# Performance work log

Hardware: AMD Instinct MI355X
Metric: run time of the kernel (lower is better)

The kernel has to match this reference:

```python
import jax, jax.numpy as jnp
import numpy as np

B, S, C = 2, 4096, 512
H = 8            # num heads
D = C // H       # head dim = 64


def setup_inputs() -> dict:
    key = jax.random.key(0)
    ks = jax.random.split(key, 5)
    s = 0.02
    return {
        "hidden_states": jax.random.normal(ks[0], (B, S, C), dtype=jnp.float32),
        "Wq": jax.random.normal(ks[1], (C, C), dtype=jnp.float32) * s,
        "Wk": jax.random.normal(ks[2], (C, C), dtype=jnp.float32) * s,
        "Wv": jax.random.normal(ks[3], (C, C), dtype=jnp.float32) * s,
        "Wo": jax.random.normal(ks[4], (C, C), dtype=jnp.float32) * s,
        "bo": jnp.zeros((C,), dtype=jnp.float32),
    }


def reference(hidden_states, Wq, Wk, Wv, Wo, bo):
    # Self-attention path of AttnProcessor (encoder_hidden_states=None,
    # no norms, no mask, residual_connection=False, rescale=1.0).
    b, s, c = hidden_states.shape
    scale = jnp.float32(D) ** -0.5
    # QKV projections (Linear, no bias as in diffusers defaults)
    q = hidden_states @ Wq.T   # [b,s,c]
    k = hidden_states @ Wk.T
    v = hidden_states @ Wv.T
    # head_to_batch_dim: [b,s,c] -> [b,s,h,d]
    q = q.reshape(b, s, H, D)
    k = k.reshape(b, s, H, D)
    v = v.reshape(b, s, H, D)
    # get_attention_scores: scaled QK^T + softmax (full O(S^2) matrix, as in source)
    scores = jnp.einsum("bqhd,bkhd->bhqk", q, k) * scale   # [b,h,s,s]
    probs = jax.nn.softmax(scores, axis=-1)
    # bmm with V, batch_to_head_dim
    out = jnp.einsum("bhqk,bkhd->bqhd", probs, v).reshape(b, s, c)
    # to_out[0] (Linear with bias); to_out[1] is Dropout (identity at eval)
    out = out @ Wo.T + bo
    return out
```

## Files before the change

### kernel.cpp

```cpp
#include <hip/hip_runtime.h>
#include <hip/hip_bf16.h>

#define BB 2
#define SS 4096
#define CC 512
#define HH 8
#define DD 64
#define MM (BB*SS)

typedef __bf16 bf16;
typedef __attribute__((ext_vector_type(8))) __bf16 bf16x8;
typedef __attribute__((ext_vector_type(4))) __bf16 bf16x4;
typedef __attribute__((ext_vector_type(4))) float f32x4;

#define LP 72
#define QSCALE 0.18033688f

__device__ __forceinline__ bf16x8 cvt8(const float4 a, const float4 b) {
  bf16x8 r;
  r[0]=(bf16)a.x; r[1]=(bf16)a.y; r[2]=(bf16)a.z; r[3]=(bf16)a.w;
  r[4]=(bf16)b.x; r[5]=(bf16)b.y; r[6]=(bf16)b.z; r[7]=(bf16)b.w;
  return r;
}

__global__ __launch_bounds__(256) void cvt_f32_bf16(
    const float* __restrict__ src, bf16* __restrict__ dst)
{
  size_t e = ((size_t)blockIdx.x * 256 + threadIdx.x) * 8;
  float4 a = ((const float4*)(src + e))[0];
  float4 b = ((const float4*)(src + e))[1];
  *(bf16x8*)(dst + e) = cvt8(a, b);
}

__global__ __launch_bounds__(256) void cvt_w(
    const float* __restrict__ Wq, const float* __restrict__ Wk,
    const float* __restrict__ Wv, bf16* __restrict__ Wb)
{
  size_t e = ((size_t)blockIdx.x * 256 + threadIdx.x) * 8;
  const int tens = (int)(e >> 18);
  const float* src = ((tens == 0) ? Wq : (tens == 1) ? Wk : Wv) + (e & 262143);
  const float sc = (tens == 0) ? QSCALE : 1.f;
  float4 a = ((const float4*)src)[0];
  float4 b = ((const float4*)src)[1];
  bf16x8 r;
  r[0]=(bf16)(a.x*sc); r[1]=(bf16)(a.y*sc); r[2]=(bf16)(a.z*sc); r[3]=(bf16)(a.w*sc);
  r[4]=(bf16)(b.x*sc); r[5]=(bf16)(b.y*sc); r[6]=(bf16)(b.z*sc); r[7]=(bf16)(b.w*sc);
  *(bf16x8*)(Wb + e) = r;
}

__global__ __launch_bounds__(256) void qkv_gemm(
    const bf16* __restrict__ Xb, const bf16* __restrict__ Wb,
    bf16* __restrict__ qp, bf16* __restrict__ kp, bf16* __restrict__ vtp)
{
  __shared__ bf16 Aa[64*LP];
  __shared__ bf16 Ab[64*LP];
  __shared__ bf16 Ba[64*LP];
  __shared__ bf16 Bb[64*LP];
  const int m0  = blockIdx.x * 128;
  const int nf0 = blockIdx.y * 128;
  const int tens = nf0 >> 9;
  const int n0 = nf0 & 511;

  const int t = threadIdx.x;
  const int w = t >> 6;
  const int lane = t & 63;
  const int l15 = lane & 15;
  const int quad = lane >> 4;
  const int srow = t >> 2;
  const int scol = (t & 3) << 4;

  f32x4 acc[2][2][4];
  #pragma unroll
  for (int mi = 0; mi < 2; ++mi)
    #pragma unroll
    for (int ni = 0; ni < 2; ++ni)
      #pragma unroll
      for (int nt = 0; nt < 4; ++nt)
        #pragma unroll
        for (int r = 0; r < 4; ++r) acc[mi][ni][nt][r] = 0.f;

  for (int k0 = 0; k0 < CC; k0 += 64) {
    __syncthreads();
    {
      const bf16* sa = Xb + (size_t)(m0 + srow) * CC + k0 + scol;
      *(bf16x8*)&Aa[srow*LP + scol]     = ((const bf16x8*)sa)[0];
      *(bf16x8*)&Aa[srow*LP + scol + 8] = ((const bf16x8*)sa)[1];
      const bf16* sb = Xb + (size_t)(m0 + 64 + srow) * CC + k0 + scol;
      *(bf16x8*)&Ab[srow*LP + scol]     = ((const bf16x8*)sb)[0];
      *(bf16x8*)&Ab[srow*LP + scol + 8] = ((const bf16x8*)sb)[1];
      const bf16* s1 = Wb + (size_t)(nf0 + srow) * CC + k0 + scol;
      *(bf16x8*)&Ba[srow*LP + scol]     = ((const bf16x8*)s1)[0];
      *(bf16x8*)&Ba[srow*LP + scol + 8] = ((const bf16x8*)s1)[1];
      const bf16* s2 = Wb + (size_t)(nf0 + 64 + srow) * CC + k0 + scol;
      *(bf16x8*)&Bb[srow*LP + scol]     = ((const bf16x8*)s2)[0];
      *(bf16x8*)&Bb[srow*LP + scol + 8] = ((const bf16x8*)s2)[1];
    }
    __syncthreads();
    #pragma unroll
    for (int c = 0; c < 2; ++c) {
      bf16x8 afa = *(const bf16x8*)&Aa[(w*16 + l15)*LP + c*32 + quad*8];
      bf16x8 afb = *(const bf16x8*)&Ab[(w*16 + l15)*LP + c*32 + quad*8];
      #pragma unroll
      for (int nt = 0; nt < 4; ++nt) {
        bf16x8 ba = *(const bf16x8*)&Ba[(nt*16 + l15)*LP + c*32 + quad*8];
        bf16x8 bb = *(const bf16x8*)&Bb[(nt*16 + l15)*LP + c*32 + quad*8];
        acc[0][0][nt] = __builtin_amdgcn_mfma_f32_16x16x32_bf16(afa, ba, acc[0][0][nt], 0, 0, 0);
        acc[1][0][nt] = __builtin_amdgcn_mfma_f32_16x16x32_bf16(afb, ba, acc[1][0][nt], 0, 0, 0);
        acc[0][1][nt] = __builtin_amdgcn_mfma_f32_16x16x32_bf16(afa, bb, acc[0][1][nt], 0, 0, 0);
        acc[1][1][nt] = __builtin_amdgcn_mfma_f32_16x16x32_bf16(afb, bb, acc[1][1][nt], 0, 0, 0);
      }
    }
  }

  bf16* plane = (tens == 0) ? qp : ((tens == 1) ? kp : vtp);
  const int c8 = (t & 7) * 8;

  auto epi = [&](const f32x4* as, int mt0, int nb) {
    const int b = mt0 >> 12, s0g = mt0 & 4095;
    const int h = nb >> 6;
    __syncthreads();
    if (tens < 2) {
      #pragma unroll
      for (int nt = 0; nt < 4; ++nt)
        #pragma unroll
        for (int r = 0; r < 4; ++r)
          Aa[(w*16 + quad*4 + r)*LP + nt*16 + l15] = (bf16)as[nt][r];
    } else {
      #pragma unroll
      for (int nt = 0; nt < 4; ++nt)
        #pragma unroll
        for (int r = 0; r < 4; ++r)
          Aa[(nt*16 + l15)*LP + w*16 + quad*4 + r] = (bf16)as[nt][r];
    }
    __syncthreads();
    #pragma unroll
    for (int i = 0; i < 2; ++i) {
      const int row = (t >> 3) + 32*i;
      bf16x8 v = *(const bf16x8*)&Aa[row*LP + c8];
      if (tens < 2) {
        *(bf16x8*)&plane[((size_t)((b*HH + h)*SS) + s0g + row)*DD + c8] = v;
      } else {
        *(bf16x8*)&plane[((size_t)((b*HH + h)*DD) + row)*SS + s0g + c8] = v;
      }
    }
  };

  epi(acc[0][0], m0,      n0);
  epi(acc[1][0], m0 + 64, n0);
  epi(acc[0][1], m0,      n0 + 64);
  epi(acc[1][1], m0 + 64, n0 + 64);
}

__global__ __launch_bounds__(512, 4) void attn_fa(
    const bf16* __restrict__ qpl, const bf16* __restrict__ kpl,
    const bf16* __restrict__ vtpl, bf16* __restrict__ aout)
{
  __shared__ __align__(16) bf16 smem[2 * 4 * 64 * LP];

  const int t = threadIdx.x;
  const int w = t >> 6;
  const int g = w >> 2;
  const int wl = w & 3;
  const int lane = t & 63;
  const int l15 = lane & 15;
  const int quad = lane >> 4;

  const int lin = blockIdx.x;
  const int bh = lin & 15;
  const int q0 = (lin >> 4) * 128;
  const size_t plane = (size_t)SS * DD;
  const bf16* Qp = qpl + (size_t)bh * plane;
  const bf16* Kp = kpl + (size_t)bh * plane;
  const bf16* Vg = vtpl + (size_t)bh * plane;

  bf16* Ktg = smem + g * (4*64*LP);
  bf16* Vtg = Ktg + 2*64*LP;

  bf16x8 qf[2][2];
  #pragma unroll
  for (int wq = 0; wq < 2; ++wq) {
    const bf16* qr = Qp + (size_t)(q0 + wl*32 + wq*16 + l15) * DD + quad*8;
    qf[wq][0] = *(const bf16x8*)qr;
    qf[wq][1] = *(const bf16x8*)(qr + 32);
  }

  f32x4 o[2][4];
  float rs[2] = {0.f, 0.f};
  #pragma unroll
  for (int wq = 0; wq < 2; ++wq)
    #pragma unroll
    for (int nt = 0; nt < 4; ++nt)
      #pragma unroll
      for (int r = 0; r < 4; ++r) o[wq][nt][r] = 0.f;

  const int t8  = t & 255;
  const int r0s = t8 >> 2;
  const int cs  = (t8 & 3) << 4;
  const int K0  = ((t8 & 1) << 3) + (((t8 >> 1) & 1) << 5);
  const int kbase = g << 11;

  bf16x8 ka0, ka1, va, vb;
  {
    ka0 = *(const bf16x8*)&Kp[(size_t)(kbase + r0s)*DD + cs];
    ka1 = *(const bf16x8*)&Kp[(size_t)(kbase + r0s)*DD + cs + 8];
    va  = *(const bf16x8*)&Vg[(size_t)r0s*SS + kbase + K0];
    vb  = *(const bf16x8*)&Vg[(size_t)r0s*SS + kbase + K0 + 16];
    *(bf16x8*)&Ktg[r0s*LP + cs]     = ka0;
    *(bf16x8*)&Ktg[r0s*LP + cs + 8] = ka1;
    bf16x8 vv;
    vv[0]=va[0]; vv[1]=va[1]; vv[2]=va[2]; vv[3]=va[3];
    vv[4]=vb[0]; vv[5]=vb[1]; vv[6]=vb[2]; vv[7]=vb[3];
    *(bf16x8*)&Vtg[r0s*LP + cs] = vv;
    vv[0]=va[4]; vv[1]=va[5]; vv[2]=va[6]; vv[3]=va[7];
    vv[4]=vb[4]; vv[5]=vb[5]; vv[6]=vb[6]; vv[7]=vb[7];
    *(bf16x8*)&Vtg[r0s*LP + cs + 8] = vv;
  }
  __syncthreads();

  for (int it = 0; it < 32; ++it) {
    const int cur = it & 1;
    if (it < 31) {
      const int kb = kbase + (it + 1) * 64;
      ka0 = *(const bf16x8*)&Kp[(size_t)(kb + r0s)*DD + cs];
      ka1 = *(const bf16x8*)&Kp[(size_t)(kb + r0s)*DD + cs + 8];
      va  = *(const bf16x8*)&Vg[(size_t)r0s*SS + kb + K0];
      vb  = *(const bf16x8*)&Vg[(size_t)r0s*SS + kb + K0 + 16];
    }

    const bf16* Ktc = Ktg + cur*(64*LP);
    const bf16* Vtc = Vtg + cur*(64*LP);

    f32x4 st[2][4];
    #pragma unroll
    for (int nt = 0; nt < 4; ++nt) {
      bf16x8 kf0 = *(const bf16x8*)&Ktc[(nt*16 + l15)*LP + quad*8];
      bf16x8 kf1 = *(const bf16x8*)&Ktc[(nt*16 + l15)*LP + 32 + quad*8];
      #pragma unroll
      for (int wq = 0; wq < 2; ++wq) {
        f32x4 z; z[0]=z[1]=z[2]=z[3]=0.f;
        z = __builtin_amdgcn_mfma_f32_16x16x32_bf16(kf0, qf[wq][0], z, 0, 0, 0);
        z = __builtin_amdgcn_mfma_f32_16x16x32_bf16(kf1, qf[wq][1], z, 0, 0, 0);
        st[wq][nt] = z;
      }
    }

    bf16x8 pb[2][2];
    #pragma unroll
    for (int wq = 0; wq < 2; ++wq) {
      float acc_s = 0.f;
      #pragma unroll
      for (int nt = 0; nt < 4; ++nt)
        #pragma unroll
        for (int r = 0; r < 4; ++r) {
          float pv = __builtin_amdgcn_exp2f(st[wq][nt][r]);
          acc_s += pv;
          pb[wq][nt >> 1][(nt & 1)*4 + r] = (bf16)pv;
        }
      rs[wq] += acc_s;
    }

    #pragma unroll
    for (int kbh = 0; kbh < 2; ++kbh) {
      #pragma unroll
      for (int nt = 0; nt < 4; ++nt) {
        bf16x8 vf = *(const bf16x8*)&Vtc[(nt*16 + l15)*LP + kbh*32 + quad*8];
        #pragma unroll
        for (int wq = 0; wq < 2; ++wq)
          o[wq][nt] = __builtin_amdgcn_mfma_f32_16x16x32_bf16(vf, pb[wq][kbh], o[wq][nt], 0, 0, 0);
      }
    }

    if (it < 31) {
      const int nxt = cur ^ 1;
      bf16* Ktn = Ktg + nxt*(64*LP);
      bf16* Vtn = Vtg + nxt*(64*LP);
      *(bf16x8*)&Ktn[r0s*LP + cs]     = ka0;
      *(bf16x8*)&Ktn[r0s*LP + cs + 8] = ka1;
      bf16x8 vv;
      vv[0]=va[0]; vv[1]=va[1]; vv[2]=va[2]; vv[3]=va[3];
      vv[4]=vb[0]; vv[5]=vb[1]; vv[6]=vb[2]; vv[7]=vb[3];
      *(bf16x8*)&Vtn[r0s*LP + cs] = vv;
      vv[0]=va[4]; vv[1]=va[5]; vv[2]=va[6]; vv[3]=va[7];
      vv[4]=vb[4]; vv[5]=vb[5]; vv[6]=vb[6]; vv[7]=vb[7];
      *(bf16x8*)&Vtn[r0s*LP + cs + 8] = vv;
      __syncthreads();
    }
  }

  __syncthreads();
  float* stash = (float*)smem;
  const int sidx = (wl*64 + lane) * 36;
  if (g == 1) {
    #pragma unroll
    for (int wq = 0; wq < 2; ++wq)
      #pragma unroll
      for (int nt = 0; nt < 4; ++nt)
        *(f32x4*)&stash[sidx + (wq*4 + nt)*4] = o[wq][nt];
    stash[sidx + 32] = rs[0];
    stash[sidx + 33] = rs[1];
  }
  __syncthreads();
  if (g == 0) {
    #pragma unroll
    for (int wq = 0; wq < 2; ++wq)
      #pragma unroll
      for (int nt = 0; nt < 4; ++nt) {
        f32x4 p = *(const f32x4*)&stash[sidx + (wq*4 + nt)*4];
        #pragma unroll
        for (int r = 0; r < 4; ++r) o[wq][nt][r] += p[r];
      }
    rs[0] += stash[sidx + 32];
    rs[1] += stash[sidx + 33];

    const int b = bh >> 3, h = bh & 7;
    #pragma unroll
    for (int wq = 0; wq < 2; ++wq) {
      float s = rs[wq];
      s += __shfl_xor(s, 16);
      s += __shfl_xor(s, 32);
      const float inv = 1.f / s;
      const size_t row = (size_t)(b*SS + q0 + wl*32 + wq*16 + l15) * CC + h*DD;
      #pragma unroll
      for (int nt = 0; nt < 4; ++nt) {
        bf16x4 ov;
        #pragma unroll
        for (int r = 0; r < 4; ++r) ov[r] = (bf16)(o[wq][nt][r] * inv);
        *(bf16x4*)&aout[row + nt*16 + quad*4] = ov;
      }
    }
  }
}

__global__ __launch_bounds__(256) void out_gemm(
    const bf16* __restrict__ A, const bf16* __restrict__ Wob,
    const float* __restrict__ bo, float* __restrict__ out)
{
  __shared__ bf16 Aa[64*LP];
  __shared__ bf16 Ab[64*LP];
  __shared__ bf16 Bt[64*LP];
  const int m0 = blockIdx.x * 128;
  const int n0 = blockIdx.y * 64;

  const int t = threadIdx.x;
  const int w = t >> 6;
  const int lane = t & 63;
  const int l15 = lane & 15;
  const int quad = lane >> 4;
  const int srow = t >> 2;
  const int scol = (t & 3) << 4;

  f32x4 aca[4], acb[4];
  #pragma unroll
  for (int i = 0; i < 4; ++i)
    #pragma unroll
    for (int j = 0; j < 4; ++j) { aca[i][j] = 0.f; acb[i][j] = 0.f; }

  for (int k0 = 0; k0 < CC; k0 += 64) {
    __syncthreads();
    {
      const bf16* sa = A + (size_t)(m0 + srow) * CC + k0 + scol;
      *(bf16x8*)&Aa[srow*LP + scol]     = ((const bf16x8*)sa)[0];
      *(bf16x8*)&Aa[srow*LP + scol + 8] = ((const bf16x8*)sa)[1];
      const bf16* sb = A + (size_t)(m0 + 64 + srow) * CC + k0 + scol;
      *(bf16x8*)&Ab[srow*LP + scol]     = ((const bf16x8*)sb)[0];
      *(bf16x8*)&Ab[srow*LP + scol + 8] = ((const bf16x8*)sb)[1];
      const bf16* s1 = Wob + (size_t)(n0 + srow) * CC + k0 + scol;
      *(bf16x8*)&Bt[srow*LP + scol]     = ((const bf16x8*)s1)[0];
      *(bf16x8*)&Bt[srow*LP + scol + 8] = ((const bf16x8*)s1)[1];
    }
    __syncthreads();
    #pragma unroll
    for (int c = 0; c < 2; ++c) {
      bf16x8 afa = *(const bf16x8*)&Aa[(w*16 + l15)*LP + c*32 + quad*8];
      bf16x8 afb = *(const bf16x8*)&Ab[(w*16 + l15)*LP + c*32 + quad*8];
      #pragma unroll
      for (int nt = 0; nt < 4; ++nt) {
        bf16x8 bfr = *(const bf16x8*)&Bt[(nt*16 + l15)*LP + c*32 + quad*8];
        aca[nt] = __builtin_amdgcn_mfma_f32_16x16x32_bf16(afa, bfr, aca[nt], 0, 0, 0);
        acb[nt] = __builtin_amdgcn_mfma_f32_16x16x32_bf16(afb, bfr, acb[nt], 0, 0, 0);
      }
    }
  }

  #pragma unroll
  for (int nt = 0; nt < 4; ++nt) {
    const int ng = n0 + nt*16 + l15;
    const float bias = bo[ng];
    #pragma unroll
    for (int r = 0; r < 4; ++r) {
      const int mga = m0 + w*16 + quad*4 + r;
      out[(size_t)mga*CC + ng] = aca[nt][r] + bias;
      const int mgb = m0 + 64 + w*16 + quad*4 + r;
      out[(size_t)mgb*CC + ng] = acb[nt][r] + bias;
    }
  }
}

extern "C" void kernel_launch(void* const* d_in, const int* in_sizes, int n_in,
                              void* d_out, int out_size, void* d_ws, size_t ws_size,
                              hipStream_t stream) {
  const float* hs = (const float*)d_in[0];
  const float* Wq = (const float*)d_in[1];
  const float* Wk = (const float*)d_in[2];
  const float* Wv = (const float*)d_in[3];
  const float* Wo = (const float*)d_in[4];
  const float* bo = (const float*)d_in[5];
  float* out = (float*)d_out;

  const size_t PE = (size_t)BB*HH*SS*DD;
  bf16* ws   = (bf16*)d_ws;
  bf16* qp   = ws;
  bf16* kp   = ws + PE;
  bf16* vtp  = ws + 2*PE;
  bf16* Xb   = ws + 3*PE;
  bf16* aout = ws + 3*PE;
  bf16* Wob  = qp;
  bf16* Wb   = ws + 4*PE;

  cvt_f32_bf16<<<dim3(2048),      256, 0, stream>>>(hs, Xb);
  cvt_w       <<<dim3(384),       256, 0, stream>>>(Wq, Wk, Wv, Wb);
  qkv_gemm<<<dim3(MM/128, 12),    256, 0, stream>>>(Xb, Wb, qp, kp, vtp);
  attn_fa <<<dim3(512),           512, 0, stream>>>(qp, kp, vtp, aout);
  cvt_f32_bf16<<<dim3(128),       256, 0, stream>>>(Wo, Wob);
  out_gemm<<<dim3(MM/128, CC/64), 256, 0, stream>>>(aout, Wob, bo, out);
}
```

Baseline: 186.7 us.

## Load V fragments directly from global memory into registers, bypassing LDS staging

Removes the shared-memory double buffer for the transposed V tile. Each lane now loads its MFMA B-operand fragments for V straight from global memory as bf16x4 pairs, split into two half-tile batches interleaved with the PV MFMAs. It also wraps the MFMA sections in s_setprio to favour matrix-issuing waves. This cuts LDS footprint and LDS write/read traffic, at the cost of narrower, less coalesced global loads whose latency is exposed within the iteration and is no longer prefetched a tile ahead.

```diff
diff --git a/kernel.cpp b/kernel.cpp
--- a/kernel.cpp
+++ b/kernel.cpp
@@ -20,6 +20,13 @@
   bf16x8 r;
   r[0]=(bf16)a.x; r[1]=(bf16)a.y; r[2]=(bf16)a.z; r[3]=(bf16)a.w;
   r[4]=(bf16)b.x; r[5]=(bf16)b.y; r[6]=(bf16)b.z; r[7]=(bf16)b.w;
+  return r;
+}
+
+__device__ __forceinline__ bf16x8 vcat(bf16x4 lo, bf16x4 hi) {
+  bf16x8 r;
+  r[0]=lo[0]; r[1]=lo[1]; r[2]=lo[2]; r[3]=lo[3];
+  r[4]=hi[0]; r[5]=hi[1]; r[6]=hi[2]; r[7]=hi[3];
   return r;
 }
 
@@ -155,7 +162,7 @@
     const bf16* __restrict__ qpl, const bf16* __restrict__ kpl,
     const bf16* __restrict__ vtpl, bf16* __restrict__ aout)
 {
-  __shared__ __align__(16) bf16 smem[2 * 4 * 64 * LP];
+  __shared__ __align__(16) bf16 smem[2 * 2 * 64 * LP];
 
   const int t = threadIdx.x;
   const int w = t >> 6;
@@ -173,8 +180,7 @@
   const bf16* Kp = kpl + (size_t)bh * plane;
   const bf16* Vg = vtpl + (size_t)bh * plane;
 
-  bf16* Ktg = smem + g * (4*64*LP);
-  bf16* Vtg = Ktg + 2*64*LP;
+  bf16* Ktg = smem + g * (2*64*LP);
 
   bf16x8 qf[2][2];
   #pragma unroll
@@ -196,41 +202,40 @@
   const int t8  = t & 255;
   const int r0s = t8 >> 2;
   const int cs  = (t8 & 3) << 4;
-  const int K0  = ((t8 & 1) << 3) + (((t8 >> 1) & 1) << 5);
   const int kbase = g << 11;
 
-  bf16x8 ka0, ka1, va, vb;
+  bf16x8 ka0, ka1;
   {
     ka0 = *(const bf16x8*)&Kp[(size_t)(kbase + r0s)*DD + cs];
     ka1 = *(const bf16x8*)&Kp[(size_t)(kbase + r0s)*DD + cs + 8];
-    va  = *(const bf16x8*)&Vg[(size_t)r0s*SS + kbase + K0];
-    vb  = *(const bf16x8*)&Vg[(size_t)r0s*SS + kbase + K0 + 16];
     *(bf16x8*)&Ktg[r0s*LP + cs]     = ka0;
     *(bf16x8*)&Ktg[r0s*LP + cs + 8] = ka1;
-    bf16x8 vv;
-    vv[0]=va[0]; vv[1]=va[1]; vv[2]=va[2]; vv[3]=va[3];
-    vv[4]=vb[0]; vv[5]=vb[1]; vv[6]=vb[2]; vv[7]=vb[3];
-    *(bf16x8*)&Vtg[r0s*LP + cs] = vv;
-    vv[0]=va[4]; vv[1]=va[5]; vv[2]=va[6]; vv[3]=va[7];
-    vv[4]=vb[4]; vv[5]=vb[5]; vv[6]=vb[6]; vv[7]=vb[7];
-    *(bf16x8*)&Vtg[r0s*LP + cs + 8] = vv;
   }
   __syncthreads();
+
+  const bf16* Vrow = Vg + (size_t)l15 * SS;
 
   for (int it = 0; it < 32; ++it) {
     const int cur = it & 1;
+    const int kb = kbase + it * 64;
     if (it < 31) {
-      const int kb = kbase + (it + 1) * 64;
-      ka0 = *(const bf16x8*)&Kp[(size_t)(kb + r0s)*DD + cs];
-      ka1 = *(const bf16x8*)&Kp[(size_t)(kb + r0s)*DD + cs + 8];
-      va  = *(const bf16x8*)&Vg[(size_t)r0s*SS + kb + K0];
-      vb  = *(const bf16x8*)&Vg[(size_t)r0s*SS + kb + K0 + 16];
+      const int kn = kb + 64;
+      ka0 = *(const bf16x8*)&Kp[(size_t)(kn + r0s)*DD + cs];
+      ka1 = *(const bf16x8*)&Kp[(size_t)(kn + r0s)*DD + cs + 8];
+    }
+
+    bf16x4 vl0[4], vh0[4];
+    #pragma unroll
+    for (int nt = 0; nt < 4; ++nt) {
+      const bf16* vp = Vrow + (size_t)(nt*16) * SS + kb + quad*4;
+      vl0[nt] = *(const bf16x4*)vp;
+      vh0[nt] = *(const bf16x4*)(vp + 16);
     }
 
     const bf16* Ktc = Ktg + cur*(64*LP);
-    const bf16* Vtc = Vtg + cur*(64*LP);
 
     f32x4 st[2][4];
+    __builtin_amdgcn_s_setprio(1);
     #pragma unroll
     for (int nt = 0; nt < 4; ++nt) {
       bf16x8 kf0 = *(const bf16x8*)&Ktc[(nt*16 + l15)*LP + quad*8];
@@ -243,6 +248,7 @@
         st[wq][nt] = z;
       }
     }
+    __builtin_amdgcn_s_setprio(0);
 
     bf16x8 pb[2][2];
     #pragma unroll
@@ -259,30 +265,38 @@
       rs[wq] += acc_s;
     }
 
-    #pragma unroll
-    for (int kbh = 0; kbh < 2; ++kbh) {
-      #pragma unroll
-      for (int nt = 0; nt < 4; ++nt) {
-        bf16x8 vf = *(const bf16x8*)&Vtc[(nt*16 + l15)*LP + kbh*32 + quad*8];
-        #pragma unroll
-        for (int wq = 0; wq < 2; ++wq)
-          o[wq][nt] = __builtin_amdgcn_mfma_f32_16x16x32_bf16(vf, pb[wq][kbh], o[wq][nt], 0, 0, 0);
-      }
-    }
+    __builtin_amdgcn_s_setprio(1);
+    #pragma unroll
+    for (int nt = 0; nt < 4; ++nt) {
+      bf16x8 vf = vcat(vl0[nt], vh0[nt]);
+      #pragma unroll
+      for (int wq = 0; wq < 2; ++wq)
+        o[wq][nt] = __builtin_amdgcn_mfma_f32_16x16x32_bf16(vf, pb[wq][0], o[wq][nt], 0, 0, 0);
+    }
+    __builtin_amdgcn_s_setprio(0);
+
+    bf16x4 vl1[4], vh1[4];
+    #pragma unroll
+    for (int nt = 0; nt < 4; ++nt) {
+      const bf16* vp = Vrow + (size_t)(nt*16) * SS + kb + 32 + quad*4;
+      vl1[nt] = *(const bf16x4*)vp;
+      vh1[nt] = *(const bf16x4*)(vp + 16);
+    }
+
+    __builtin_amdgcn_s_setprio(1);
+    #pragma unroll
+    for (int nt = 0; nt < 4; ++nt) {
+      bf16x8 vf = vcat(vl1[nt], vh1[nt]);
+      #pragma unroll
+      for (int wq = 0; wq < 2; ++wq)
+        o[wq][nt] = __builtin_amdgcn_mfma_f32_16x16x32_bf16(vf, pb[wq][1], o[wq][nt], 0, 0, 0);
+    }
+    __builtin_amdgcn_s_setprio(0);
 
     if (it < 31) {
-      const int nxt = cur ^ 1;
-      bf16* Ktn = Ktg + nxt*(64*LP);
-      bf16* Vtn = Vtg + nxt*(64*LP);
+      bf16* Ktn = Ktg + (cur ^ 1)*(64*LP);
       *(bf16x8*)&Ktn[r0s*LP + cs]     = ka0;
       *(bf16x8*)&Ktn[r0s*LP + cs + 8] = ka1;
-      bf16x8 vv;
-      vv[0]=va[0]; vv[1]=va[1]; vv[2]=va[2]; vv[3]=va[3];
-      vv[4]=vb[0]; vv[5]=vb[1]; vv[6]=vb[2]; vv[7]=vb[3];
-      *(bf16x8*)&Vtn[r0s*LP + cs] = vv;
-      vv[0]=va[4]; vv[1]=va[5]; vv[2]=va[6]; vv[3]=va[7];
-      vv[4]=vb[4]; vv[5]=vb[5]; vv[6]=vb[6]; vv[7]=vb[7];
-      *(bf16x8*)&Vtn[r0s*LP + cs + 8] = vv;
       __syncthreads();
     }
   }
```

Result: slower. 388.4 us (+108.0%).

## Split exp/PV into halves, compute row sums via MFMA with ones, add setprio

Applied to the files above, without the earlier changes.

The softmax row sum is now produced by an extra MFMA against a ones vector on the bf16-rounded probabilities, replacing the scalar adds and the cross-lane shuffles at the end. The exp and PV stages are split into two key halves so the exponentials of the second half can overlap with the MFMAs of the first. s_setprio hints raise wave priority around the MFMA blocks. This adds four extra MFMAs per iteration, and the denominators are now summed from bf16-rounded values rather than fp32 ones.

```diff
diff --git a/kernel.cpp b/kernel.cpp
--- a/kernel.cpp
+++ b/kernel.cpp
@@ -185,13 +185,20 @@
   }
 
   f32x4 o[2][4];
-  float rs[2] = {0.f, 0.f};
-  #pragma unroll
-  for (int wq = 0; wq < 2; ++wq)
+  f32x4 osum[2];
+  #pragma unroll
+  for (int wq = 0; wq < 2; ++wq) {
     #pragma unroll
     for (int nt = 0; nt < 4; ++nt)
       #pragma unroll
       for (int r = 0; r < 4; ++r) o[wq][nt][r] = 0.f;
+    #pragma unroll
+    for (int r = 0; r < 4; ++r) osum[wq][r] = 0.f;
+  }
+
+  bf16x8 ones;
+  #pragma unroll
+  for (int i = 0; i < 8; ++i) ones[i] = (bf16)1.0f;
 
   const int t8  = t & 255;
   const int r0s = t8 >> 2;
@@ -220,17 +227,18 @@
   for (int it = 0; it < 32; ++it) {
     const int cur = it & 1;
     if (it < 31) {
-      const int kb = kbase + (it + 1) * 64;
-      ka0 = *(const bf16x8*)&Kp[(size_t)(kb + r0s)*DD + cs];
-      ka1 = *(const bf16x8*)&Kp[(size_t)(kb + r0s)*DD + cs + 8];
-      va  = *(const bf16x8*)&Vg[(size_t)r0s*SS + kb + K0];
-      vb  = *(const bf16x8*)&Vg[(size_t)r0s*SS + kb + K0 + 16];
+      const int kn = kbase + (it + 1) * 64;
+      ka0 = *(const bf16x8*)&Kp[(size_t)(kn + r0s)*DD + cs];
+      ka1 = *(const bf16x8*)&Kp[(size_t)(kn + r0s)*DD + cs + 8];
+      va  = *(const bf16x8*)&Vg[(size_t)r0s*SS + kn + K0];
+      vb  = *(const bf16x8*)&Vg[(size_t)r0s*SS + kn + K0 + 16];
     }
 
     const bf16* Ktc = Ktg + cur*(64*LP);
     const bf16* Vtc = Vtg + cur*(64*LP);
 
     f32x4 st[2][4];
+    __builtin_amdgcn_s_setprio(1);
     #pragma unroll
     for (int nt = 0; nt < 4; ++nt) {
       bf16x8 kf0 = *(const bf16x8*)&Ktc[(nt*16 + l15)*LP + quad*8];
@@ -243,32 +251,51 @@
         st[wq][nt] = z;
       }
     }
-
-    bf16x8 pb[2][2];
-    #pragma unroll
-    for (int wq = 0; wq < 2; ++wq) {
-      float acc_s = 0.f;
-      #pragma unroll
-      for (int nt = 0; nt < 4; ++nt)
-        #pragma unroll
-        for (int r = 0; r < 4; ++r) {
-          float pv = __builtin_amdgcn_exp2f(st[wq][nt][r]);
-          acc_s += pv;
-          pb[wq][nt >> 1][(nt & 1)*4 + r] = (bf16)pv;
-        }
-      rs[wq] += acc_s;
-    }
-
-    #pragma unroll
-    for (int kbh = 0; kbh < 2; ++kbh) {
-      #pragma unroll
-      for (int nt = 0; nt < 4; ++nt) {
-        bf16x8 vf = *(const bf16x8*)&Vtc[(nt*16 + l15)*LP + kbh*32 + quad*8];
-        #pragma unroll
-        for (int wq = 0; wq < 2; ++wq)
-          o[wq][nt] = __builtin_amdgcn_mfma_f32_16x16x32_bf16(vf, pb[wq][kbh], o[wq][nt], 0, 0, 0);
-      }
-    }
+    __builtin_amdgcn_s_setprio(0);
+
+    bf16x8 pb0[2];
+    #pragma unroll
+    for (int wq = 0; wq < 2; ++wq)
+      #pragma unroll
+      for (int nt = 0; nt < 2; ++nt)
+        #pragma unroll
+        for (int r = 0; r < 4; ++r)
+          pb0[wq][(nt & 1)*4 + r] = (bf16)__builtin_amdgcn_exp2f(st[wq][nt][r]);
+
+    __builtin_amdgcn_s_setprio(1);
+    #pragma unroll
+    for (int nt = 0; nt < 4; ++nt) {
+      bf16x8 vf = *(const bf16x8*)&Vtc[(nt*16 + l15)*LP + quad*8];
+      #pragma unroll
+      for (int wq = 0; wq < 2; ++wq)
+        o[wq][nt] = __builtin_amdgcn_mfma_f32_16x16x32_bf16(vf, pb0[wq], o[wq][nt], 0, 0, 0);
+    }
+    #pragma unroll
+    for (int wq = 0; wq < 2; ++wq)
+      osum[wq] = __builtin_amdgcn_mfma_f32_16x16x32_bf16(ones, pb0[wq], osum[wq], 0, 0, 0);
+    __builtin_amdgcn_s_setprio(0);
+
+    bf16x8 pb1[2];
+    #pragma unroll
+    for (int wq = 0; wq < 2; ++wq)
+      #pragma unroll
+      for (int nt = 2; nt < 4; ++nt)
+        #pragma unroll
+        for (int r = 0; r < 4; ++r)
+          pb1[wq][(nt & 1)*4 + r] = (bf16)__builtin_amdgcn_exp2f(st[wq][nt][r]);
+
+    __builtin_amdgcn_s_setprio(1);
+    #pragma unroll
+    for (int nt = 0; nt < 4; ++nt) {
+      bf16x8 vf = *(const bf16x8*)&Vtc[(nt*16 + l15)*LP + 32 + quad*8];
+      #pragma unroll
+      for (int wq = 0; wq < 2; ++wq)
+        o[wq][nt] = __builtin_amdgcn_mfma_f32_16x16x32_bf16(vf, pb1[wq], o[wq][nt], 0, 0, 0);
+    }
+    #pragma unroll
+    for (int wq = 0; wq < 2; ++wq)
+      osum[wq] = __builtin_amdgcn_mfma_f32_16x16x32_bf16(ones, pb1[wq], osum[wq], 0, 0, 0);
+    __builtin_amdgcn_s_setprio(0);
 
     if (it < 31) {
       const int nxt = cur ^ 1;
@@ -296,8 +323,8 @@
       #pragma unroll
       for (int nt = 0; nt < 4; ++nt)
         *(f32x4*)&stash[sidx + (wq*4 + nt)*4] = o[wq][nt];
-    stash[sidx + 32] = rs[0];
-    stash[sidx + 33] = rs[1];
+    stash[sidx + 32] = osum[0][0];
+    stash[sidx + 33] = osum[1][0];
   }
   __syncthreads();
   if (g == 0) {
@@ -309,16 +336,13 @@
         #pragma unroll
         for (int r = 0; r < 4; ++r) o[wq][nt][r] += p[r];
       }
-    rs[0] += stash[sidx + 32];
-    rs[1] += stash[sidx + 33];
+    const float s0 = osum[0][0] + stash[sidx + 32];
+    const float s1 = osum[1][0] + stash[sidx + 33];
 
     const int b = bh >> 3, h = bh & 7;
     #pragma unroll
     for (int wq = 0; wq < 2; ++wq) {
-      float s = rs[wq];
-      s += __shfl_xor(s, 16);
-      s += __shfl_xor(s, 32);
-      const float inv = 1.f / s;
+      const float inv = 1.f / (wq == 0 ? s0 : s1);
       const size_t row = (size_t)(b*SS + q0 + wl*32 + wq*16 + l15) * CC + h*DD;
       #pragma unroll
       for (int nt = 0; nt < 4; ++nt) {
```

After: 187.1 us. No clear change (+0.2%).
